# Kernel tuning notes

Hardware: AMD Instinct MI355X
Metric: run time of the kernel (lower is better)

The kernel has to match this reference:

```python
import jax, jax.numpy as jnp
import numpy as np

B, L, N, D = 8, 512, 64, 1024  # batch, seq_len, num_entities, hidden_size


def setup_inputs() -> dict:
    key = jax.random.key(0)
    ks = jax.random.split(key, 18)
    g = lambda i, shape: jax.random.normal(ks[i], shape, dtype=jnp.float32) * 0.02
    inp = {
        "h": jax.random.normal(ks[0], (B, L, D), dtype=jnp.float32),
        "span_idx": jax.random.randint(ks[1], (B, N, 2), 0, L, dtype=jnp.int64),
        # SpanMarkerV0 project_start: Linear(D,2D) -> ReLU -> Linear(2D,D)
        "Ws1": g(2, (D, 2 * D)), "bs1": jnp.zeros((2 * D,), jnp.float32),
        "Ws2": g(3, (2 * D, D)), "bs2": jnp.zeros((D,), jnp.float32),
        # SpanMarkerV0 project_end
        "We1": g(4, (D, 2 * D)), "be1": jnp.zeros((2 * D,), jnp.float32),
        "We2": g(5, (2 * D, D)), "be2": jnp.zeros((D,), jnp.float32),
        # SpanMarkerV0 out_project: Linear(2D, 2D)
        "Wo": g(6, (2 * D, 2 * D)), "bo": jnp.zeros((2 * D,), jnp.float32),
        # relationship_projector: Linear(4D,2D) -> ReLU -> Linear(2D,D)
        "Wr1": g(7, (4 * D, 2 * D)), "br1": jnp.zeros((2 * D,), jnp.float32),
        "Wr2": g(8, (2 * D, D)), "br2": jnp.zeros((D,), jnp.float32),
    }
    return inp


def reference(h, span_idx, Ws1, bs1, Ws2, bs2, We1, be1, We2, be2, Wo, bo,
              Wr1, br1, Wr2, br2):
    # ---- SpanMarkerV0 entity encoder (dropout = identity at inference) ----
    start_proj = jax.nn.relu(h @ Ws1 + bs1) @ Ws2 + bs2  # (B, L, D)
    end_proj = jax.nn.relu(h @ We1 + be1) @ We2 + be2    # (B, L, D)
    bidx = jnp.arange(h.shape[0])[:, None]
    start_rep = start_proj[bidx, span_idx[:, :, 0]]      # (B, N, D)
    end_rep = end_proj[bidx, span_idx[:, :, 1]]          # (B, N, D)
    cat = jax.nn.relu(jnp.concatenate([start_rep, end_rep], axis=-1))
    entity_reps = cat @ Wo + bo                          # (B, N, 2D)

    # ---- pairwise relationship projector ----
    # torch: cat([tile_i, tile_j], -1) @ Wr1  ==  e_i @ Wr1[:2D] + e_j @ Wr1[2D:]
    half = Wr1.shape[0] // 2
    hi = entity_reps @ Wr1[:half]                        # (B, N, 2D)
    hj = entity_reps @ Wr1[half:]                        # (B, N, 2D)
    hidden = jax.nn.relu(hi[:, :, None, :] + hj[:, None, :, :] + br1)  # (B,N,N,2D)
    return hidden @ Wr2 + br2                            # (B, N, N, D)
```

## Files before the change

kernel.cpp:

```cpp
#include <hip/hip_runtime.h>
#include <hip/hip_bf16.h>

constexpr int Lseq = 512;
constexpr int Nsp  = 64;
constexpr int Dm   = 1024;
constexpr int D2   = 2048;

typedef __attribute__((ext_vector_type(8))) short short8;
typedef __attribute__((ext_vector_type(4))) float floatx4;
typedef unsigned short u16;
typedef unsigned int   u32;

__device__ __forceinline__ u32 f2bf(float x) {
    u32 u = __float_as_uint(x);
    return (u + 0x7fffu + ((u >> 16) & 1u)) >> 16;
}
__device__ __forceinline__ float bf2f(u32 hbits) {
    return __uint_as_float(hbits << 16);
}
__device__ __forceinline__ u32 pk2(float x0, float x1) {
    __hip_bfloat162 bb = __float22bfloat162_rn(make_float2(x0, x1));
    u32 r; __builtin_memcpy(&r, &bb, 4); return r;
}

__global__ __launch_bounds__(256)
void gather_split(const float* __restrict__ h, const int* __restrict__ span,
                  u16* __restrict__ g_hi, u16* __restrict__ g_lo)
{
    const int row = blockIdx.x, which = blockIdx.y;
    const int b = row >> 6;
    const int idx = span[row * 2 + which];
    const float4* src = (const float4*)(h + ((size_t)b * Lseq + idx) * Dm);
    float4 v = src[threadIdx.x];
    u32 h01 = pk2(v.x, v.y), h23 = pk2(v.z, v.w);
    u32 l01 = pk2(v.x - bf2f(h01 & 0xffffu), v.y - bf2f(h01 >> 16));
    u32 l23 = pk2(v.z - bf2f(h23 & 0xffffu), v.w - bf2f(h23 >> 16));
    size_t off = ((size_t)which * 512 + row) * Dm + (size_t)threadIdx.x * 4;
    *(uint2*)(g_hi + off) = make_uint2(h01, h23);
    *(uint2*)(g_lo + off) = make_uint2(l01, l23);
}

__global__ __launch_bounds__(256)
void gather_rows(const float* __restrict__ h, const int* __restrict__ span,
                 float* __restrict__ gs, float* __restrict__ ge)
{
    const int row = blockIdx.x, which = blockIdx.y;
    const int b = row >> 6;
    const int idx = span[row * 2 + which];
    const float4* src = (const float4*)(h + ((size_t)b * Lseq + idx) * Dm);
    float4* dst = (float4*)((which ? ge : gs) + (size_t)row * Dm);
    dst[threadIdx.x] = src[threadIdx.x];
}

struct TransJobs {
    const float* src[8];
    u16* dh[8];
    u16* dl[8];
    int K[8], N[8], tiles[8];
};

__global__ __launch_bounds__(256)
void transpose_split(TransJobs J)
{
    __shared__ float T[64][65];
    int b = blockIdx.x, j = 0;
    while (b >= J.tiles[j]) { b -= J.tiles[j]; ++j; }
    const float* src = J.src[j];
    const int K = J.K[j], N = J.N[j];
    const int tk = K >> 6;
    const int k0 = (b % tk) * 64, n0 = (b / tk) * 64;
    const int t = threadIdx.x, c = t & 63, r4 = t >> 6;
#pragma unroll
    for (int s = 0; s < 16; ++s) {
        int r = r4 * 16 + s;
        T[r][c] = src[(size_t)(k0 + r) * N + n0 + c];
    }
    __syncthreads();
    u16* dh = J.dh[j];
    u16* dl = J.dl[j];
#pragma unroll
    for (int s = 0; s < 16; ++s) {
        int n = r4 * 16 + s;
        float v = T[c][n];
        u32 hv = f2bf(v);
        dh[(size_t)(n0 + n) * K + k0 + c] = (u16)hv;
        if (dl) dl[(size_t)(n0 + n) * K + k0 + c] = (u16)f2bf(v - bf2f(hv));
    }
}

struct GemmP {
    const u16 *ah0, *ah1, *al0, *al1;
    const u16 *wh0, *wh1, *wl0, *wl1;
    const float *b0, *b1;
    float *of0, *of1;
    u16 *oh0, *oh1, *ol0, *ol1;
    int K, ldc, coloff1;
};

template<bool RELU, bool BIAS, bool SPLIT_OUT>
__global__ __launch_bounds__(256)
void gemm_split(GemmP P)
{
    __shared__ __align__(16) u16 As_h[64 * 32];
    __shared__ __align__(16) u16 As_l[64 * 32];
    __shared__ __align__(16) u16 Bs_h[64 * 32];
    __shared__ __align__(16) u16 Bs_l[64 * 32];

    const int tid = threadIdx.x, w = tid >> 6, l = tid & 63;
    const int lr = l & 15, lq = l >> 4;
    const int z = blockIdx.z;
    const int m0 = blockIdx.x * 64, n0 = blockIdx.y * 64;
    const int K = P.K;

    const u16* ah = z ? P.ah1 : P.ah0;
    const u16* al = z ? P.al1 : P.al0;
    const u16* wh = z ? P.wh1 : P.wh0;
    const u16* wl = z ? P.wl1 : P.wl0;

    const u16* src; u16* ldst;
    if      (w == 0) { src = ah + (size_t)m0 * K; ldst = As_h; }
    else if (w == 1) { src = al + (size_t)m0 * K; ldst = As_l; }
    else if (w == 2) { src = wh + (size_t)n0 * K; ldst = Bs_h; }
    else             { src = wl + (size_t)n0 * K; ldst = Bs_l; }
    const u16* sl = src + (size_t)(l >> 2) * K + (size_t)(l & 3) * 8;

    floatx4 acc[4];
#pragma unroll
    for (int nt = 0; nt < 4; ++nt) acc[nt] = (floatx4){0.f, 0.f, 0.f, 0.f};

    for (int k0 = 0; k0 < K; k0 += 32) {
        __syncthreads();
#pragma unroll
        for (int i = 0; i < 4; ++i)
            __builtin_amdgcn_global_load_lds(
                (const __attribute__((address_space(1))) u32*)(sl + (size_t)i * 16 * K + k0),
                (__attribute__((address_space(3))) u32*)(ldst + i * 512), 16, 0, 0);
        __syncthreads();

        const int ar = (w * 16 + lr) * 32 + lq * 8;
        short8 fah = *(const short8*)&As_h[ar];
        short8 fal = *(const short8*)&As_l[ar];
#pragma unroll
        for (int nt = 0; nt < 4; ++nt) {
            const int brd = (nt * 16 + lr) * 32 + lq * 8;
            short8 fbh = *(const short8*)&Bs_h[brd];
            short8 fbl = *(const short8*)&Bs_l[brd];
            acc[nt] = __builtin_amdgcn_mfma_f32_16x16x32_bf16(fah, fbh, acc[nt], 0, 0, 0);
            acc[nt] = __builtin_amdgcn_mfma_f32_16x16x32_bf16(fal, fbh, acc[nt], 0, 0, 0);
            acc[nt] = __builtin_amdgcn_mfma_f32_16x16x32_bf16(fah, fbl, acc[nt], 0, 0, 0);
        }
    }

    const float* bias = z ? P.b1 : P.b0;
    const int colb = n0 + (z ? P.coloff1 : 0);
    float bv[4];
    if (BIAS) {
#pragma unroll
        for (int nt = 0; nt < 4; ++nt) bv[nt] = bias[n0 + nt * 16 + lr];
    }
#pragma unroll
    for (int nt = 0; nt < 4; ++nt) {
#pragma unroll
        for (int r = 0; r < 4; ++r) {
            float x = acc[nt][r];
            if (BIAS) x += bv[nt];
            if (RELU) x = fmaxf(x, 0.f);
            const int m = m0 + w * 16 + lq * 4 + r;
            const size_t oidx = (size_t)m * P.ldc + colb + nt * 16 + lr;
            if (SPLIT_OUT) {
                u16* oh = z ? P.oh1 : P.oh0;
                u16* ol = z ? P.ol1 : P.ol0;
                u32 hv = f2bf(x);
                oh[oidx] = (u16)hv;
                ol[oidx] = (u16)f2bf(x - bf2f(hv));
            } else {
                float* of = z ? P.of1 : P.of0;
                of[oidx] = x;
            }
        }
    }
}

template<bool RELU, bool BIAS>
__global__ __launch_bounds__(256)
void gemm_f32(const float* __restrict__ A, int lda,
              const float* __restrict__ W, int ldw,
              const float* __restrict__ bias,
              float* __restrict__ C, int ldc, int K)
{
    __shared__ float As[16][64];
    __shared__ float Ws[16][64];
    const int tid = threadIdx.x;
    const int tx = tid & 15, ty = tid >> 4;
    const int m0 = blockIdx.x * 64, n0 = blockIdx.y * 64;
    const int la_c = tid & 15, la_r = tid >> 4;
    const int lw_n = tid & 63, lw_k = tid >> 6;
    float acc[4][4] = {};
    for (int k0 = 0; k0 < K; k0 += 16) {
#pragma unroll
        for (int s = 0; s < 4; ++s) {
            int m = la_r + 16 * s;
            As[la_c][m] = A[(size_t)(m0 + m) * lda + k0 + la_c];
        }
#pragma unroll
        for (int s = 0; s < 4; ++s) {
            int k = lw_k + 4 * s;
            Ws[k][lw_n] = W[(size_t)(k0 + k) * ldw + n0 + lw_n];
        }
        __syncthreads();
#pragma unroll
        for (int kk = 0; kk < 16; ++kk) {
            float a4[4], w4[4];
            *(float4*)a4 = *(const float4*)&As[kk][ty * 4];
            *(float4*)w4 = *(const float4*)&Ws[kk][tx * 4];
#pragma unroll
            for (int i = 0; i < 4; ++i)
#pragma unroll
                for (int j = 0; j < 4; ++j)
                    acc[i][j] = fmaf(a4[i], w4[j], acc[i][j]);
        }
        __syncthreads();
    }
#pragma unroll
    for (int i = 0; i < 4; ++i) {
        float4 v; float* vp = (float*)&v;
#pragma unroll
        for (int j = 0; j < 4; ++j) {
            float x = acc[i][j];
            if (BIAS) x += bias[n0 + tx * 4 + j];
            if (RELU) x = fmaxf(x, 0.f);
            vp[j] = x;
        }
        *(float4*)&C[(size_t)(m0 + ty * 4 + i) * ldc + n0 + tx * 4] = v;
    }
}

__global__ __launch_bounds__(256, 3)
void big_mfma(const float* __restrict__ hi, const float* __restrict__ hj,
              const float* __restrict__ br1, const u16* __restrict__ Wt,
              const float* __restrict__ br2, float* __restrict__ out)
{
    __shared__ float hiP[2][D2];
    __shared__ __align__(16) u16 Asb[128 * 32];
    __shared__ __align__(16) u16 Bsb[128 * 32];

    const int tid = threadIdx.x;
    const int p = blockIdx.x, n0 = blockIdx.y * 128;
    const int b = p >> 5, bi0 = p * 2;

    {
        const float4* h0 = (const float4*)(hi + (size_t)bi0 * D2);
        const float4* h1 = (const float4*)(hi + (size_t)(bi0 + 1) * D2);
        const float4* br = (const float4*)br1;
        float4* d0 = (float4*)hiP[0];
        float4* d1 = (float4*)hiP[1];
        for (int v = tid; v < 512; v += 256) {
            float4 bb = br[v];
            float4 a = h0[v];
            a.x += bb.x; a.y += bb.y; a.z += bb.z; a.w += bb.w;
            d0[v] = a;
            float4 c = h1[v];
            c.x += bb.x; c.y += bb.y; c.z += bb.z; c.w += bb.w;
            d1[v] = c;
        }
    }

    const int w = tid >> 6, l = tid & 63;
    const int wm = w & 1, wn = w >> 1;
    const int lr = l & 15, lq = l >> 4;

    const int c4 = l & 3;
    const int r0 = w * 32 + (l >> 2);
    const int r1 = r0 + 16;
    const int sel0 = r0 >> 6, j0 = r0 & 63;
    const int sel1 = r1 >> 6, j1 = r1 & 63;
    const float* hj0 = hj + ((size_t)b * 64 + j0) * D2 + c4 * 8;
    const float* hj1 = hj + ((size_t)b * 64 + j1) * D2 + c4 * 8;

    floatx4 acc[4][4];
#pragma unroll
    for (int mt = 0; mt < 4; ++mt)
#pragma unroll
        for (int nt = 0; nt < 4; ++nt)
            acc[mt][nt] = (floatx4){0.f, 0.f, 0.f, 0.f};

    for (int k0 = 0; k0 < D2; k0 += 32) {
        __syncthreads();

        {
            float4 a0 = *(const float4*)(hj0 + k0);
            float4 a1 = *(const float4*)(hj0 + k0 + 4);
            float4 h0 = *(const float4*)&hiP[sel0][k0 + c4 * 8];
            float4 h1 = *(const float4*)&hiP[sel0][k0 + c4 * 8 + 4];
            u32 u0 = pk2(fmaxf(a0.x + h0.x, 0.f), fmaxf(a0.y + h0.y, 0.f));
            u32 u1 = pk2(fmaxf(a0.z + h0.z, 0.f), fmaxf(a0.w + h0.w, 0.f));
            u32 u2 = pk2(fmaxf(a1.x + h1.x, 0.f), fmaxf(a1.y + h1.y, 0.f));
            u32 u3 = pk2(fmaxf(a1.z + h1.z, 0.f), fmaxf(a1.w + h1.w, 0.f));
            *(uint4*)&Asb[r0 * 32 + c4 * 8] = make_uint4(u0, u1, u2, u3);

            float4 b0 = *(const float4*)(hj1 + k0);
            float4 b1 = *(const float4*)(hj1 + k0 + 4);
            float4 g0 = *(const float4*)&hiP[sel1][k0 + c4 * 8];
            float4 g1 = *(const float4*)&hiP[sel1][k0 + c4 * 8 + 4];
            u32 v0 = pk2(fmaxf(b0.x + g0.x, 0.f), fmaxf(b0.y + g0.y, 0.f));
            u32 v1 = pk2(fmaxf(b0.z + g0.z, 0.f), fmaxf(b0.w + g0.w, 0.f));
            u32 v2 = pk2(fmaxf(b1.x + g1.x, 0.f), fmaxf(b1.y + g1.y, 0.f));
            u32 v3 = pk2(fmaxf(b1.z + g1.z, 0.f), fmaxf(b1.w + g1.w, 0.f));
            *(uint4*)&Asb[r1 * 32 + c4 * 8] = make_uint4(v0, v1, v2, v3);
        }

#pragma unroll
        for (int c = 0; c < 2; ++c) {
            const u16* g = Wt + (size_t)(n0 + w * 32 + c * 16 + (l >> 2)) * D2
                              + k0 + (l & 3) * 8;
            u16* lp = Bsb + (w * 2048 + c * 1024) / 2;
            __builtin_amdgcn_global_load_lds(
                (const __attribute__((address_space(1))) u32*)g,
                (__attribute__((address_space(3))) u32*)lp, 16, 0, 0);
        }

        __syncthreads();

        short8 af[4], bfr[4];
#pragma unroll
        for (int mt = 0; mt < 4; ++mt)
            af[mt] = *(const short8*)&Asb[(wm * 64 + mt * 16 + lr) * 32 + lq * 8];
#pragma unroll
        for (int nt = 0; nt < 4; ++nt)
            bfr[nt] = *(const short8*)&Bsb[(wn * 64 + nt * 16 + lr) * 32 + lq * 8];
#pragma unroll
        for (int mt = 0; mt < 4; ++mt)
#pragma unroll
            for (int nt = 0; nt < 4; ++nt)
                acc[mt][nt] = __builtin_amdgcn_mfma_f32_16x16x32_bf16(
                    af[mt], bfr[nt], acc[mt][nt], 0, 0, 0);
    }

    float bias[4];
#pragma unroll
    for (int nt = 0; nt < 4; ++nt)
        bias[nt] = br2[n0 + wn * 64 + nt * 16 + lr];

#pragma unroll
    for (int mt = 0; mt < 4; ++mt) {
        const int mbase = wm * 64 + mt * 16 + lq * 4;
#pragma unroll
        for (int r = 0; r < 4; ++r) {
            const int mm = mbase + r;
            const int sel = mm >> 6, j = mm & 63;
            float* orow = out + (((size_t)(bi0 + sel) * 64 + j) * Dm) + n0 + wn * 64;
#pragma unroll
            for (int nt = 0; nt < 4; ++nt)
                orow[nt * 16 + lr] = acc[mt][nt][r] + bias[nt];
        }
    }
}

extern "C" void kernel_launch(void* const* d_in, const int* in_sizes, int n_in,
                              void* d_out, int out_size, void* d_ws, size_t ws_size,
                              hipStream_t stream) {
    const float* h    = (const float*)d_in[0];
    const int*   span = (const int*)  d_in[1];
    const float* Ws1  = (const float*)d_in[2];
    const float* bs1  = (const float*)d_in[3];
    const float* Ws2  = (const float*)d_in[4];
    const float* bs2  = (const float*)d_in[5];
    const float* We1  = (const float*)d_in[6];
    const float* be1  = (const float*)d_in[7];
    const float* We2  = (const float*)d_in[8];
    const float* be2  = (const float*)d_in[9];
    const float* Wo   = (const float*)d_in[10];
    const float* bo   = (const float*)d_in[11];
    const float* Wr1  = (const float*)d_in[12];
    const float* br1  = (const float*)d_in[13];
    const float* Wr2  = (const float*)d_in[14];
    const float* br2  = (const float*)d_in[15];
    float* out = (float*)d_out;

    dim3 blk(256);
    const size_t REQUIRED = (size_t)120 << 20;

    if (ws_size >= REQUIRED) {
        char* W = (char*)d_ws;
        size_t off = 0;
        auto alloc = [&](size_t bytes) { char* q = W + off; off += bytes; return q; };

        u16* W1t_h = (u16*)alloc((size_t)2 * 2048 * 1024 * 2);
        u16* W1t_l = (u16*)alloc((size_t)2 * 2048 * 1024 * 2);
        u16* W2t_h = (u16*)alloc((size_t)2 * 1024 * 2048 * 2);
        u16* W2t_l = (u16*)alloc((size_t)2 * 1024 * 2048 * 2);
        u16* Wot_h = (u16*)alloc((size_t)2048 * 2048 * 2);
        u16* Wot_l = (u16*)alloc((size_t)2048 * 2048 * 2);
        u16* Wr1t_h = (u16*)alloc((size_t)2 * 2048 * 2048 * 2);
        u16* Wr1t_l = (u16*)alloc((size_t)2 * 2048 * 2048 * 2);
        u16* Wr2t_h = (u16*)alloc((size_t)1024 * 2048 * 2);
        u16* gs_h  = (u16*)alloc((size_t)2 * 512 * 1024 * 2);
        u16* gs_l  = (u16*)alloc((size_t)2 * 512 * 1024 * 2);
        u16* t1_h  = (u16*)alloc((size_t)2 * 512 * 2048 * 2);
        u16* t1_l  = (u16*)alloc((size_t)2 * 512 * 2048 * 2);
        u16* cat_h = (u16*)alloc((size_t)512 * 2048 * 2);
        u16* cat_l = (u16*)alloc((size_t)512 * 2048 * 2);
        u16* ent_h = (u16*)alloc((size_t)512 * 2048 * 2);
        u16* ent_l = (u16*)alloc((size_t)512 * 2048 * 2);
        float* hif = (float*)alloc((size_t)512 * 2048 * 4);
        float* hjf = (float*)alloc((size_t)512 * 2048 * 4);

        TransJobs J;
        J.src[0] = Ws1;  J.dh[0] = W1t_h;                J.dl[0] = W1t_l;                J.K[0] = 1024; J.N[0] = 2048; J.tiles[0] = 512;
        J.src[1] = We1;  J.dh[1] = W1t_h + 2048 * 1024;  J.dl[1] = W1t_l + 2048 * 1024;  J.K[1] = 1024; J.N[1] = 2048; J.tiles[1] = 512;
        J.src[2] = Ws2;  J.dh[2] = W2t_h;                J.dl[2] = W2t_l;                J.K[2] = 2048; J.N[2] = 1024; J.tiles[2] = 512;
        J.src[3] = We2;  J.dh[3] = W2t_h + 1024 * 2048;  J.dl[3] = W2t_l + 1024 * 2048;  J.K[3] = 2048; J.N[3] = 1024; J.tiles[3] = 512;
        J.src[4] = Wo;   J.dh[4] = Wot_h;                J.dl[4] = Wot_l;                J.K[4] = 2048; J.N[4] = 2048; J.tiles[4] = 1024;
        J.src[5] = Wr1;  J.dh[5] = Wr1t_h;               J.dl[5] = Wr1t_l;               J.K[5] = 2048; J.N[5] = 2048; J.tiles[5] = 1024;
        J.src[6] = Wr1 + (size_t)2048 * 2048;
                         J.dh[6] = Wr1t_h + (size_t)2048 * 2048; J.dl[6] = Wr1t_l + (size_t)2048 * 2048;
                                                                          J.K[6] = 2048; J.N[6] = 2048; J.tiles[6] = 1024;
        J.src[7] = Wr2;  J.dh[7] = Wr2t_h;               J.dl[7] = nullptr;              J.K[7] = 2048; J.N[7] = 1024; J.tiles[7] = 512;
        transpose_split<<<dim3(5632), blk, 0, stream>>>(J);

        gather_split<<<dim3(512, 2), blk, 0, stream>>>(h, span, gs_h, gs_l);

        GemmP p1 = {};
        p1.ah0 = gs_h; p1.ah1 = gs_h + 512 * 1024;
        p1.al0 = gs_l; p1.al1 = gs_l + 512 * 1024;
        p1.wh0 = W1t_h; p1.wh1 = W1t_h + 2048 * 1024;
        p1.wl0 = W1t_l; p1.wl1 = W1t_l + 2048 * 1024;
        p1.b0 = bs1; p1.b1 = be1;
        p1.oh0 = t1_h; p1.oh1 = t1_h + 512 * 2048;
        p1.ol0 = t1_l; p1.ol1 = t1_l + 512 * 2048;
        p1.K = 1024; p1.ldc = 2048; p1.coloff1 = 0;
        gemm_split<true, true, true><<<dim3(8, 32, 2), blk, 0, stream>>>(p1);

        GemmP p2 = {};
        p2.ah0 = t1_h; p2.ah1 = t1_h + 512 * 2048;
        p2.al0 = t1_l; p2.al1 = t1_l + 512 * 2048;
        p2.wh0 = W2t_h; p2.wh1 = W2t_h + 1024 * 2048;
        p2.wl0 = W2t_l; p2.wl1 = W2t_l + 1024 * 2048;
        p2.b0 = bs2; p2.b1 = be2;
        p2.oh0 = cat_h; p2.oh1 = cat_h;
        p2.ol0 = cat_l; p2.ol1 = cat_l;
        p2.K = 2048; p2.ldc = 2048; p2.coloff1 = 1024;
        gemm_split<true, true, true><<<dim3(8, 16, 2), blk, 0, stream>>>(p2);

        GemmP p3 = {};
        p3.ah0 = cat_h; p3.al0 = cat_l;
        p3.wh0 = Wot_h; p3.wl0 = Wot_l;
        p3.b0 = bo;
        p3.oh0 = ent_h; p3.ol0 = ent_l;
        p3.K = 2048; p3.ldc = 2048; p3.coloff1 = 0;
        gemm_split<false, true, true><<<dim3(8, 32, 1), blk, 0, stream>>>(p3);

        GemmP p4 = {};
        p4.ah0 = ent_h; p4.ah1 = ent_h;
        p4.al0 = ent_l; p4.al1 = ent_l;
        p4.wh0 = Wr1t_h; p4.wh1 = Wr1t_h + (size_t)2048 * 2048;
        p4.wl0 = Wr1t_l; p4.wl1 = Wr1t_l + (size_t)2048 * 2048;
        p4.of0 = hif; p4.of1 = hjf;
        p4.K = 2048; p4.ldc = 2048; p4.coloff1 = 0;
        gemm_split<false, false, false><<<dim3(8, 32, 2), blk, 0, stream>>>(p4);

        big_mfma<<<dim3(256, 8), blk, 0, stream>>>(hif, hjf, br1, Wr2t_h, br2, out);
    } else {
        u16* Wt = (u16*)d_ws;
        float* ws  = (float*)((char*)d_ws + (size_t)Dm * D2 * 2);
        float* gs  = ws;
        float* ge  = gs  + 512 * Dm;
        float* t1  = ge  + 512 * Dm;
        float* cat = t1  + 512 * D2;
        float* ent = cat + 512 * D2;
        float* hi  = ent + 512 * D2;
        float* hj  = hi  + 512 * D2;

        TransJobs J = {};
        J.src[0] = Wr2; J.dh[0] = Wt; J.dl[0] = nullptr;
        J.K[0] = 2048; J.N[0] = 1024; J.tiles[0] = 512;
        transpose_split<<<dim3(512), blk, 0, stream>>>(J);

        gather_rows<<<dim3(512, 2), blk, 0, stream>>>(h, span, gs, ge);
        gemm_f32<true,  true><<<dim3(8, 32), blk, 0, stream>>>(gs, Dm, Ws1, D2, bs1, t1, D2, Dm);
        gemm_f32<true,  true><<<dim3(8, 16), blk, 0, stream>>>(t1, D2, Ws2, Dm, bs2, cat, D2, D2);
        gemm_f32<true,  true><<<dim3(8, 32), blk, 0, stream>>>(ge, Dm, We1, D2, be1, t1, D2, Dm);
        gemm_f32<true,  true><<<dim3(8, 16), blk, 0, stream>>>(t1, D2, We2, Dm, be2, cat + Dm, D2, D2);
        gemm_f32<false, true><<<dim3(8, 32), blk, 0, stream>>>(cat, D2, Wo, D2, bo, ent, D2, D2);
        gemm_f32<false, false><<<dim3(8, 32), blk, 0, stream>>>(ent, D2, Wr1, D2, nullptr, hi, D2, D2);
        gemm_f32<false, false><<<dim3(8, 32), blk, 0, stream>>>(ent, D2, Wr1 + (size_t)D2 * D2, D2, nullptr, hj, D2, D2);
        big_mfma<<<dim3(256, 8), blk, 0, stream>>>(hi, hj, br1, Wt, br2, out);
    }
}
```

Before: 556.1 us.

## Widen big_mfma to 512 threads and 256-col tiles with hj register prefetch

The final pairwise GEMM kernel now runs 512-thread blocks (8 waves), each covering 128 rows by 256 output columns, which halves the grid along N. The relu(hi+hj) A-tile is built once per block for twice as many columns, so that elementwise work and the hj reloads are amortised further. The A tile moves to a k-quarter-major LDS layout, and the next k-step's hj values are prefetched into registers after the barrier. s_setprio is raised around the MFMA loop. The cost is larger blocks, more registers per thread, and possible occupancy limits under the new launch bounds.

```diff
diff --git a/kernel.cpp b/kernel.cpp
--- a/kernel.cpp
+++ b/kernel.cpp
@@ -235,18 +235,27 @@
     }
 }
 
-__global__ __launch_bounds__(256, 3)
+__global__ __launch_bounds__(512, 4)
 void big_mfma(const float* __restrict__ hi, const float* __restrict__ hj,
               const float* __restrict__ br1, const u16* __restrict__ Wt,
               const float* __restrict__ br2, float* __restrict__ out)
 {
     __shared__ float hiP[2][D2];
-    __shared__ __align__(16) u16 Asb[128 * 32];
-    __shared__ __align__(16) u16 Bsb[128 * 32];
+    __shared__ __align__(16) u16 Asb[4 * 128 * 8];
+    __shared__ __align__(16) u16 Bsb[256 * 32];
 
     const int tid = threadIdx.x;
-    const int p = blockIdx.x, n0 = blockIdx.y * 128;
+    const int p = blockIdx.x, n0 = blockIdx.y * 256;
     const int b = p >> 5, bi0 = p * 2;
+
+    const int rowA = tid >> 2, kq = tid & 3;
+    const int selA = rowA >> 6, jA = rowA & 63;
+    const float* hjrow = hj + ((size_t)b * 64 + jA) * D2 + kq * 8;
+    u16* astore = Asb + (kq * 128 + rowA) * 8;
+    const float* hip = hiP[selA] + kq * 8;
+
+    float4 pf0 = *(const float4*)(hjrow);
+    float4 pf1 = *(const float4*)(hjrow + 4);
 
     {
         const float4* h0 = (const float4*)(hi + (size_t)bi0 * D2);
@@ -254,29 +263,20 @@
         const float4* br = (const float4*)br1;
         float4* d0 = (float4*)hiP[0];
         float4* d1 = (float4*)hiP[1];
-        for (int v = tid; v < 512; v += 256) {
-            float4 bb = br[v];
-            float4 a = h0[v];
-            a.x += bb.x; a.y += bb.y; a.z += bb.z; a.w += bb.w;
-            d0[v] = a;
-            float4 c = h1[v];
-            c.x += bb.x; c.y += bb.y; c.z += bb.z; c.w += bb.w;
-            d1[v] = c;
-        }
+        const int v = tid;
+        float4 bb = br[v];
+        float4 a = h0[v];
+        a.x += bb.x; a.y += bb.y; a.z += bb.z; a.w += bb.w;
+        d0[v] = a;
+        float4 c = h1[v];
+        c.x += bb.x; c.y += bb.y; c.z += bb.z; c.w += bb.w;
+        d1[v] = c;
     }
 
     const int w = tid >> 6, l = tid & 63;
     const int wm = w & 1, wn = w >> 1;
     const int lr = l & 15, lq = l >> 4;
 
-    const int c4 = l & 3;
-    const int r0 = w * 32 + (l >> 2);
-    const int r1 = r0 + 16;
-    const int sel0 = r0 >> 6, j0 = r0 & 63;
-    const int sel1 = r1 >> 6, j1 = r1 & 63;
-    const float* hj0 = hj + ((size_t)b * 64 + j0) * D2 + c4 * 8;
-    const float* hj1 = hj + ((size_t)b * 64 + j1) * D2 + c4 * 8;
-
     floatx4 acc[4][4];
 #pragma unroll
     for (int mt = 0; mt < 4; ++mt)
@@ -288,32 +288,20 @@
         __syncthreads();
 
         {
-            float4 a0 = *(const float4*)(hj0 + k0);
-            float4 a1 = *(const float4*)(hj0 + k0 + 4);
-            float4 h0 = *(const float4*)&hiP[sel0][k0 + c4 * 8];
-            float4 h1 = *(const float4*)&hiP[sel0][k0 + c4 * 8 + 4];
-            u32 u0 = pk2(fmaxf(a0.x + h0.x, 0.f), fmaxf(a0.y + h0.y, 0.f));
-            u32 u1 = pk2(fmaxf(a0.z + h0.z, 0.f), fmaxf(a0.w + h0.w, 0.f));
-            u32 u2 = pk2(fmaxf(a1.x + h1.x, 0.f), fmaxf(a1.y + h1.y, 0.f));
-            u32 u3 = pk2(fmaxf(a1.z + h1.z, 0.f), fmaxf(a1.w + h1.w, 0.f));
-            *(uint4*)&Asb[r0 * 32 + c4 * 8] = make_uint4(u0, u1, u2, u3);
-
-            float4 b0 = *(const float4*)(hj1 + k0);
-            float4 b1 = *(const float4*)(hj1 + k0 + 4);
-            float4 g0 = *(const float4*)&hiP[sel1][k0 + c4 * 8];
-            float4 g1 = *(const float4*)&hiP[sel1][k0 + c4 * 8 + 4];
-            u32 v0 = pk2(fmaxf(b0.x + g0.x, 0.f), fmaxf(b0.y + g0.y, 0.f));
-            u32 v1 = pk2(fmaxf(b0.z + g0.z, 0.f), fmaxf(b0.w + g0.w, 0.f));
-            u32 v2 = pk2(fmaxf(b1.x + g1.x, 0.f), fmaxf(b1.y + g1.y, 0.f));
-            u32 v3 = pk2(fmaxf(b1.z + g1.z, 0.f), fmaxf(b1.w + g1.w, 0.f));
-            *(uint4*)&Asb[r1 * 32 + c4 * 8] = make_uint4(v0, v1, v2, v3);
+            float4 h0 = *(const float4*)(hip + k0);
+            float4 h1 = *(const float4*)(hip + k0 + 4);
+            u32 u0 = pk2(fmaxf(pf0.x + h0.x, 0.f), fmaxf(pf0.y + h0.y, 0.f));
+            u32 u1 = pk2(fmaxf(pf0.z + h0.z, 0.f), fmaxf(pf0.w + h0.w, 0.f));
+            u32 u2 = pk2(fmaxf(pf1.x + h1.x, 0.f), fmaxf(pf1.y + h1.y, 0.f));
+            u32 u3 = pk2(fmaxf(pf1.z + h1.z, 0.f), fmaxf(pf1.w + h1.w, 0.f));
+            *(uint4*)astore = make_uint4(u0, u1, u2, u3);
         }
 
 #pragma unroll
         for (int c = 0; c < 2; ++c) {
             const u16* g = Wt + (size_t)(n0 + w * 32 + c * 16 + (l >> 2)) * D2
                               + k0 + (l & 3) * 8;
-            u16* lp = Bsb + (w * 2048 + c * 1024) / 2;
+            u16* lp = Bsb + (w * 32 + c * 16) * 32;
             __builtin_amdgcn_global_load_lds(
                 (const __attribute__((address_space(1))) u32*)g,
                 (__attribute__((address_space(3))) u32*)lp, 16, 0, 0);
@@ -321,19 +309,26 @@
 
         __syncthreads();
 
+        if (k0 + 32 < D2) {
+            pf0 = *(const float4*)(hjrow + k0 + 32);
+            pf1 = *(const float4*)(hjrow + k0 + 36);
+        }
+
         short8 af[4], bfr[4];
 #pragma unroll
         for (int mt = 0; mt < 4; ++mt)
-            af[mt] = *(const short8*)&Asb[(wm * 64 + mt * 16 + lr) * 32 + lq * 8];
+            af[mt] = *(const short8*)&Asb[lq * 1024 + (wm * 64 + mt * 16 + lr) * 8];
 #pragma unroll
         for (int nt = 0; nt < 4; ++nt)
             bfr[nt] = *(const short8*)&Bsb[(wn * 64 + nt * 16 + lr) * 32 + lq * 8];
+        __builtin_amdgcn_s_setprio(1);
 #pragma unroll
         for (int mt = 0; mt < 4; ++mt)
 #pragma unroll
             for (int nt = 0; nt < 4; ++nt)
                 acc[mt][nt] = __builtin_amdgcn_mfma_f32_16x16x32_bf16(
                     af[mt], bfr[nt], acc[mt][nt], 0, 0, 0);
+        __builtin_amdgcn_s_setprio(0);
     }
 
     float bias[4];
@@ -459,7 +454,7 @@
         p4.K = 2048; p4.ldc = 2048; p4.coloff1 = 0;
         gemm_split<false, false, false><<<dim3(8, 32, 2), blk, 0, stream>>>(p4);
 
-        big_mfma<<<dim3(256, 8), blk, 0, stream>>>(hif, hjf, br1, Wr2t_h, br2, out);
+        big_mfma<<<dim3(256, 4), dim3(512), 0, stream>>>(hif, hjf, br1, Wr2t_h, br2, out);
     } else {
         u16* Wt = (u16*)d_ws;
         float* ws  = (float*)((char*)d_ws + (size_t)Dm * D2 * 2);
@@ -484,6 +479,6 @@
         gemm_f32<false, true><<<dim3(8, 32), blk, 0, stream>>>(cat, D2, Wo, D2, bo, ent, D2, D2);
         gemm_f32<false, false><<<dim3(8, 32), blk, 0, stream>>>(ent, D2, Wr1, D2, nullptr, hi, D2, D2);
         gemm_f32<false, false><<<dim3(8, 32), blk, 0, stream>>>(ent, D2, Wr1 + (size_t)D2 * D2, D2, nullptr, hj, D2, D2);
-        big_mfma<<<dim3(256, 8), blk, 0, stream>>>(hi, hj, br1, Wt, br2, out);
-    }
-}
+        big_mfma<<<dim3(256, 4), dim3(512), 0, stream>>>(hi, hj, br1, Wt, br2, out);
+    }
+}
```

Result: faster. 539.1 us (-3.1%).
